# Kernel optimization log

Measured on AMD Instinct MI355X. Metric: run time of the kernel, lower is better.

Reference implementation:

```python
import jax, jax.numpy as jnp
import numpy as np

N = 250000           # points
B = 2                # batch size
GX, GY, GZ = 256, 256, 32   # voxel grid
SCALES = (2, 4, 6, 8)
CIN = 64             # input_channels
CR = 64              # reduce_channels
CH = CR // 2         # hidden = reduce_channels // 2
COUT = 64            # output_channels


def _cdiv(a, b):
    return -(-a // b)


def setup_inputs() -> dict:
    key = jax.random.key(0)
    ks = jax.random.split(key, 16)
    x = jax.random.normal(ks[0], (N, CIN), jnp.float32)
    bcol = jax.random.randint(ks[1], (N, 1), 0, B)
    xy = jax.random.randint(ks[2], (N, 2), 0, GX)
    z = jax.random.randint(ks[3], (N, 1), 0, GZ)
    coords = jnp.concatenate([bcol, xy, z], axis=1).astype(jnp.int32)
    coords_inv = jnp.arange(N, dtype=jnp.int32)

    def lin(k, fan_in, shape):
        return jax.random.normal(k, shape, jnp.float32) / np.sqrt(fan_in)

    return {
        "x": x,
        "coords": coords,
        "coords_inv": coords_inv,
        "W_red": lin(ks[4], CIN, (CIN, CR)),
        "b_red": jnp.zeros((CR,), jnp.float32),
        "W_pool": lin(ks[5], CR, (len(SCALES), CR, CH)),   # fc_list
        "b_pool": jnp.zeros((len(SCALES), CH), jnp.float32),
        "W_att": lin(ks[6], CH, (len(SCALES), CH, CH)),    # fcs
        "b_att": jnp.zeros((len(SCALES), CH), jnp.float32),
        "W_z": lin(ks[7], CH, (CH, CH)),                   # self.fc (no bias)
        "W_out": lin(ks[8], CH, (CH, CR)),                 # out_fc (no bias)
        "W_l1": lin(ks[9], 2 * CR, (2 * CR, CR)),          # linear_output[0] (no bias)
        "W_l2": lin(ks[10], CR, (CR, COUT)),               # linear_output[2]
        "b_l2": jnp.zeros((COUT,), jnp.float32),
    }


def reference(x, coords, coords_inv, W_red, b_red, W_pool, b_pool,
              W_att, b_att, W_z, W_out, W_l1, W_l2, b_l2):
    # feature_reduce + ReLU
    red = jax.nn.relu(x @ W_red + b_red)              # [N, CR]
    bidx = coords[:, 0].astype(jnp.int32)
    cxyz = coords[:, 1:]

    outs = []
    for j, ps in enumerate(SCALES):
        gx, gy, gz = _cdiv(GX, ps), _cdiv(GY, ps), _cdiv(GZ, ps)
        q = cxyz // ps                                 # quantized coords
        seg = ((bidx * gx + q[:, 0]) * gy + q[:, 1]) * gz + q[:, 2]
        ns = B * gx * gy * gz
        # scatter_mean over voxels at this scale
        sums = jax.ops.segment_sum(red, seg, num_segments=ns)
        cnt = jax.ops.segment_sum(jnp.ones((N, 1), red.dtype), seg, num_segments=ns)
        fkm = sums / jnp.maximum(cnt, 1.0)             # [ns, CR]
        # per-scale MLP then gather back to points
        att = jax.nn.relu(fkm @ W_pool[j] + b_pool[j])[seg]   # [N, CH]
        outs.append(att)

    sf = jnp.stack(outs, axis=1)                       # [N, S, CH]
    feat_Z = jax.nn.relu(sf.sum(axis=1) @ W_z)         # [N, CH]
    att_vecs = jnp.stack([feat_Z @ W_att[j] + b_att[j] for j in range(len(SCALES))], axis=1)
    att_vecs = jax.nn.sigmoid(att_vecs)                # [N, S, CH]
    scale_features = (sf * att_vecs).sum(axis=1) @ W_out   # [N, CR]
    out_f = jnp.concatenate([red, scale_features], axis=1)  # [N, 2*CR]
    proj = jax.nn.relu(out_f @ W_l1) @ W_l2 + b_l2     # [N, COUT]
    return proj[coords_inv]
```

## Files before the change

kernel.cpp:

```cpp
#include <hip/hip_runtime.h>
#include <hip/hip_bf16.h>

#define SEG1 524288
#define SEG2 589824
#define SEG3 612012
#define SEGT 620204

#define K2B0 8192
#define K2B1 9216
#define K2B2 9563
#define K2BT 9691

#define PYRB12 10968

#define SUMS_OFF 32000000ull
#define CNT_OFF  111386112ull
#define ATT_OFF  113866928ull
#define WQ_OFF   153560064ull

typedef __attribute__((ext_vector_type(8))) __bf16 bf16x8;
typedef __attribute__((ext_vector_type(4))) float  f32x4;

__device__ __forceinline__ float bf2f(unsigned short u) {
    union { unsigned int i; float f; } v; v.i = ((unsigned int)u) << 16; return v.f;
}
__device__ __forceinline__ unsigned short f2bf(float f) {
    union { float f; unsigned int i; } v; v.f = f;
    unsigned int r = v.i + 0x7FFF + ((v.i >> 16) & 1);
    return (unsigned short)(r >> 16);
}
__device__ __forceinline__ void atom_pk_bf16(unsigned int* addr, unsigned int pk) {
    asm volatile("global_atomic_pk_add_bf16 %0, %1, off" :: "v"(addr), "v"(pk) : "memory");
}

__device__ __forceinline__ int seg0_of(int b, int cx, int cy, int cz) {
    return ((b*128 + (cx>>1))*128 + (cy>>1))*16 + (cz>>1);
}
__device__ __forceinline__ void seg4(int b, int cx, int cy, int cz, int* s) {
    s[0] =        ((b*128 + (cx>>1))*128 + (cy>>1))*16 + (cz>>1);
    s[1] = SEG1 + ((b*64  + (cx>>2))*64  + (cy>>2))*8  + (cz>>2);
    s[2] = SEG2 + ((b*43  + (cx/6 ))*43  + (cy/6 ))*6  + (cz/6 );
    s[3] = SEG3 + ((b*32  + (cx>>3))*32  + (cy>>3))*4  + (cz>>3);
}

__global__ __launch_bounds__(256) void k0_wprep(
    const float* __restrict__ W_red, const float* __restrict__ W_pool,
    const float* __restrict__ W_z, const float* __restrict__ W_att,
    const float* __restrict__ W_out, const float* __restrict__ W_l1,
    const float* __restrict__ W_l2, char* __restrict__ wq)
{
    int g = blockIdx.x*256 + threadIdx.x;
    if (g < 4096) {
        int idx = g; int k = idx>>6, c = idx&63;
        int byte = (((c<<7)+(k<<1)) ^ ((c&7)<<4));
        *(unsigned short*)(wq + byte) = f2bf(W_red[idx]);
    } else if (g < 12288) {
        int idx = g - 4096; int j = idx>>11, r2 = idx&2047, k = r2>>5, c = r2&31;
        int byte = j*4096 + (((c<<7)+(k<<1)) ^ ((c&7)<<4));
        *(unsigned short*)(wq + 8192 + byte) = f2bf(W_pool[idx]);
    } else if (g < 13312) {
        int idx = g - 12288; int k = idx>>5, c = idx&31;
        *(unsigned short*)(wq + 24576 + ((k>>3)*32+c)*16 + (k&7)*2) = f2bf(W_z[idx]);
    } else if (g < 17408) {
        int idx = g - 13312; int j = idx>>10, rem = idx&1023, k = rem>>5, c = rem&31;
        *(unsigned short*)(wq + 26624 + j*2048 + ((k>>3)*32+c)*16 + (k&7)*2) = f2bf(W_att[idx]);
    } else if (g < 19456) {
        int idx = g - 17408; int k = idx>>6, c = idx&63;
        *(unsigned short*)(wq + 34816 + ((k>>3)*64+c)*16 + (k&7)*2) = f2bf(W_out[idx]);
    } else if (g < 27648) {
        int idx = g - 19456; int k = idx>>6, c = idx&63;
        int byte = (((c<<8)+(k<<1)) ^ ((c&7)<<4));
        *(unsigned short*)(wq + 38912 + byte) = f2bf(W_l1[idx]);
    } else if (g < 31744) {
        int idx = g - 27648; int k = idx>>6, c = idx&63;
        int byte = (((c<<7)+(k<<1)) ^ ((c&7)<<4));
        *(unsigned short*)(wq + 55296 + byte) = f2bf(W_l2[idx]);
    }
}

__global__ __launch_bounds__(256) void k1_mfma(
    const float* __restrict__ x, const int* __restrict__ coords,
    const char* __restrict__ wq, const float* __restrict__ b_red,
    unsigned int* __restrict__ red32, unsigned int* __restrict__ sums_pk,
    float* __restrict__ cnt, int n)
{
    __shared__ uint4 Ax4[512];
    __shared__ uint4 Bw4[512];
    __shared__ uint4 Rt4[512];
    __shared__ int segl[64];
    char* Ax = (char*)Ax4; char* Bw = (char*)Bw4; char* Rt = (char*)Rt4;

    int t = threadIdx.x;
    int i0 = blockIdx.x * 64;

    if (t < 64) {
        int r = i0 + t;
        if (r < n) {
            int4 cv = *(const int4*)&coords[(size_t)r*4];
            int s0 = seg0_of(cv.x, cv.y, cv.z, cv.w);
            segl[t] = s0;
            unsafeAtomicAdd(&cnt[s0], 1.f);
        } else segl[t] = -1;
    }
    {
        const uint4* src = (const uint4*)wq;
        for (int idx = t; idx < 512; idx += 256) Bw4[idx] = src[idx];
    }
    #pragma unroll
    for (int i2 = 0; i2 < 2; ++i2) {
        int idx = i2*256 + t;
        int row = idx >> 3, kc = idx & 7;
        int r = i0 + row;
        unsigned short u[8];
        if (r < n) {
            float4 v0 = *(const float4*)&x[(size_t)r*64 + kc*8];
            float4 v1 = *(const float4*)&x[(size_t)r*64 + kc*8 + 4];
            u[0]=f2bf(v0.x); u[1]=f2bf(v0.y); u[2]=f2bf(v0.z); u[3]=f2bf(v0.w);
            u[4]=f2bf(v1.x); u[5]=f2bf(v1.y); u[6]=f2bf(v1.z); u[7]=f2bf(v1.w);
        } else {
            #pragma unroll
            for (int q = 0; q < 8; ++q) u[q] = 0;
        }
        int byte = ((row << 7) + (kc << 4)) ^ ((row & 7) << 4);
        *(uint4*)(Ax + byte) = *(const uint4*)u;
    }
    __syncthreads();

    int lane = t & 63, wv = t >> 6;
    int hi = lane >> 4, lo = lane & 15;
    int arow = wv*16 + lo;

    f32x4 acc[4];
    #pragma unroll
    for (int nt = 0; nt < 4; ++nt) acc[nt] = (f32x4){0.f,0.f,0.f,0.f};
    #pragma unroll
    for (int kk = 0; kk < 2; ++kk) {
        int abyte = ((arow << 7) + ((kk*4 + hi) << 4)) ^ ((arow & 7) << 4);
        bf16x8 af = *(const bf16x8*)(Ax + abyte);
        #pragma unroll
        for (int nt = 0; nt < 4; ++nt) {
            int brow = nt*16 + lo;
            int bbyte = ((brow << 7) + ((kk*4 + hi) << 4)) ^ ((brow & 7) << 4);
            bf16x8 bf = *(const bf16x8*)(Bw + bbyte);
            acc[nt] = __builtin_amdgcn_mfma_f32_16x16x32_bf16(af, bf, acc[nt], 0, 0, 0);
        }
    }
    #pragma unroll
    for (int nt = 0; nt < 4; ++nt) {
        int col = nt*16 + lo;
        float bb = b_red[col];
        #pragma unroll
        for (int r = 0; r < 4; ++r) {
            int row = wv*16 + hi*4 + r;
            int byte = ((row << 7) + (col << 1)) ^ ((row & 7) << 4);
            *(unsigned short*)(Rt + byte) = f2bf(fmaxf(acc[nt][r] + bb, 0.f));
        }
    }
    __syncthreads();

    #pragma unroll
    for (int i2 = 0; i2 < 2; ++i2) {
        int idx = i2*256 + t;
        int row = idx >> 3, ck = idx & 7;
        int r = i0 + row;
        if (r < n) {
            int byte = ((row << 7) + (ck << 4)) ^ ((row & 7) << 4);
            *(uint4*)&red32[(size_t)r*32 + ck*4] = *(const uint4*)(Rt + byte);
        }
    }
    {
        int half = t >> 5, c = t & 31;
        #pragma unroll
        for (int i2 = 0; i2 < 8; ++i2) {
            int p = i2*8 + half;
            int s0_ = segl[p];
            if (s0_ >= 0) {
                int byte = ((p << 7) + (c << 2)) ^ ((p & 7) << 4);
                unsigned int pk = *(const unsigned int*)(Rt + byte);
                atom_pk_bf16(&sums_pk[(size_t)s0_*32 + c], pk);
            }
        }
    }
    asm volatile("s_waitcnt vmcnt(0)" ::: "memory");
}

__global__ __launch_bounds__(256) void k_pyramid(
    unsigned int* __restrict__ sums_pk, float* __restrict__ cnt)
{
    int t = threadIdx.x;
    int lane = t & 31;
    int cg = blockIdx.x * 8 + (t >> 5);

    float a0 = 0.f, a1 = 0.f, ca = 0.f;
    int outSeg = -1;

    if (cg < 65536) {
        int r1 = cg;
        int qz = r1 & 7, qy = (r1 >> 3) & 63, qx = (r1 >> 9) & 63, b = r1 >> 15;
        #pragma unroll
        for (int d = 0; d < 8; ++d) {
            int x2 = 2*qx + (d>>2), y2 = 2*qy + ((d>>1)&1), z2 = 2*qz + (d&1);
            int child = ((b*128 + x2)*128 + y2)*16 + z2;
            unsigned int v = sums_pk[(size_t)child*32 + lane];
            a0 += bf2f((unsigned short)(v & 0xffff));
            a1 += bf2f((unsigned short)(v >> 16));
            if (lane == 0) ca += cnt[child];
        }
        outSeg = SEG1 + r1;
    } else {
        int r2 = cg - 65536;
        if (r2 < 22188) {
            int z6 = r2 % 6; int tmp = r2 / 6;
            int y6 = tmp % 43; tmp /= 43;
            int x6 = tmp % 43; int b = tmp / 43;
            for (int dx = 0; dx < 3; ++dx) {
                int x2 = 3*x6 + dx; if (x2 >= 128) break;
                for (int dy = 0; dy < 3; ++dy) {
                    int y2 = 3*y6 + dy; if (y2 >= 128) break;
                    for (int dz = 0; dz < 3; ++dz) {
                        int z2 = 3*z6 + dz; if (z2 >= 16) break;
                        int child = ((b*128 + x2)*128 + y2)*16 + z2;
                        unsigned int v = sums_pk[(size_t)child*32 + lane];
                        a0 += bf2f((unsigned short)(v & 0xffff));
                        a1 += bf2f((unsigned short)(v >> 16));
                        if (lane == 0) ca += cnt[child];
                    }
                }
            }
            outSeg = SEG2 + r2;
        }
    }

    if (outSeg >= 0) {
        unsigned int pk = (unsigned int)f2bf(a0) | ((unsigned int)f2bf(a1) << 16);
        sums_pk[(size_t)outSeg*32 + lane] = pk;
        if (lane == 0) cnt[outSeg] = ca;
    }
}

__global__ __launch_bounds__(256) void k_pyr3(
    unsigned int* __restrict__ sums_pk, float* __restrict__ cnt)
{
    int t = threadIdx.x;
    int lane = t & 31;
    int r3 = blockIdx.x * 8 + (t >> 5);
    int z8 = r3 & 3, y8 = (r3 >> 2) & 31, x8 = (r3 >> 7) & 31, b = r3 >> 12;
    float a0 = 0.f, a1 = 0.f, ca = 0.f;
    #pragma unroll
    for (int d = 0; d < 8; ++d) {
        int qx = 2*x8 + (d>>2), qy = 2*y8 + ((d>>1)&1), qz = 2*z8 + (d&1);
        int child = SEG1 + ((b*64 + qx)*64 + qy)*8 + qz;
        unsigned int v = sums_pk[(size_t)child*32 + lane];
        a0 += bf2f((unsigned short)(v & 0xffff));
        a1 += bf2f((unsigned short)(v >> 16));
        if (lane == 0) ca += cnt[child];
    }
    unsigned int pk = (unsigned int)f2bf(a0) | ((unsigned int)f2bf(a1) << 16);
    sums_pk[(size_t)(SEG3 + r3)*32 + lane] = pk;
    if (lane == 0) cnt[SEG3 + r3] = ca;
}

__global__ __launch_bounds__(256) void k2_mfma(
    const unsigned int* __restrict__ sums_pk, const float* __restrict__ cnt,
    const char* __restrict__ wq, const float* __restrict__ b_pool,
    unsigned short* __restrict__ att)
{
    __shared__ uint4 As4[512];
    __shared__ uint4 Bs4[256];
    char* As = (char*)As4; char* Bs = (char*)Bs4;

    int t = threadIdx.x;
    int bid = blockIdx.x;
    int j, rel;
    if (bid < K2B0)      { j = 0; rel = bid; }
    else if (bid < K2B1) { j = 1; rel = bid - K2B0; }
    else if (bid < K2B2) { j = 2; rel = bid - K2B1; }
    else                 { j = 3; rel = bid - K2B2; }
    const int segStartT[4] = {0, SEG1, SEG2, SEG3};
    const int segEndT[4]   = {SEG1, SEG2, SEG3, SEGT};
    int s0 = segStartT[j] + rel * 64;
    int sEnd = segEndT[j];

    {
        const uint4* src = (const uint4*)(wq + 8192 + j*4096);
        for (int idx = t; idx < 256; idx += 256) Bs4[idx] = src[idx];
    }
    #pragma unroll
    for (int i = 0; i < 4; ++i) {
        int idx = i*256 + t;
        int p = idx >> 4, c4 = idx & 15;
        int s = s0 + p;
        unsigned int lo = 0, hi2 = 0; float inv = 0.f;
        if (s < sEnd) {
            uint2 v = *(const uint2*)&sums_pk[(size_t)s*32 + c4*2];
            lo = v.x; hi2 = v.y;
            inv = 1.f / fmaxf(cnt[s], 1.f);
        }
        unsigned short u[4] = { f2bf(bf2f((unsigned short)(lo & 0xffff))*inv),
                                f2bf(bf2f((unsigned short)(lo >> 16))*inv),
                                f2bf(bf2f((unsigned short)(hi2 & 0xffff))*inv),
                                f2bf(bf2f((unsigned short)(hi2 >> 16))*inv) };
        int byte = ((p << 7) + (c4 << 3)) ^ ((p & 7) << 4);
        *(uint2*)(As + byte) = *(const uint2*)u;
    }
    __syncthreads();

    int lane = t & 63, wv = t >> 6;
    int hi = lane >> 4, lo = lane & 15;
    int arow = wv*16 + lo;

    f32x4 acc[2];
    acc[0] = (f32x4){0.f,0.f,0.f,0.f};
    acc[1] = (f32x4){0.f,0.f,0.f,0.f};
    #pragma unroll
    for (int kk = 0; kk < 2; ++kk) {
        int abyte = ((arow << 7) + ((kk*4 + hi) << 4)) ^ ((arow & 7) << 4);
        bf16x8 af = *(const bf16x8*)(As + abyte);
        #pragma unroll
        for (int nt = 0; nt < 2; ++nt) {
            int brow = nt*16 + lo;
            int bbyte = ((brow << 7) + ((kk*4 + hi) << 4)) ^ ((brow & 7) << 4);
            bf16x8 bf = *(const bf16x8*)(Bs + bbyte);
            acc[nt] = __builtin_amdgcn_mfma_f32_16x16x32_bf16(af, bf, acc[nt], 0, 0, 0);
        }
    }
    #pragma unroll
    for (int nt = 0; nt < 2; ++nt) {
        int col = nt*16 + lo;
        float bp = b_pool[j*32 + col];
        #pragma unroll
        for (int r = 0; r < 4; ++r) {
            int s = s0 + wv*16 + hi*4 + r;
            if (s < sEnd) att[(size_t)s*32 + col] = f2bf(fmaxf(acc[nt][r] + bp, 0.f));
        }
    }
}

__global__ __launch_bounds__(256) void k3a_mfma(
    const int* __restrict__ coords, const unsigned short* __restrict__ att,
    const char* __restrict__ wq, const float* __restrict__ b_att,
    unsigned short* __restrict__ sfeat, int n)
{
    __shared__ uint4 wcomb4[896];
    __shared__ unsigned short sf[8192];
    __shared__ unsigned short AsWs[2048];
    __shared__ unsigned short Fz[2048];
    __shared__ int segl[64][4];
    char* wzp  = (char*)wcomb4;
    char* wattp = (char*)wcomb4 + 2048;
    char* wotp = (char*)wcomb4 + 10240;

    int t = threadIdx.x;
    int i0 = blockIdx.x * 64;
    if (t < 64) {
        int r = i0 + t; if (r >= n) r = n - 1;
        int sg[4]; seg4(coords[r*4], coords[r*4+1], coords[r*4+2], coords[r*4+3], sg);
        segl[t][0]=sg[0]; segl[t][1]=sg[1]; segl[t][2]=sg[2]; segl[t][3]=sg[3];
    }
    {
        const uint4* src = (const uint4*)(wq + 24576);
        for (int idx = t; idx < 896; idx += 256) wcomb4[idx] = src[idx];
    }
    __syncthreads();

    #pragma unroll
    for (int i = 0; i < 4; ++i) {
        int idx = i*256 + t;
        int p = idx >> 4, j = (idx >> 2) & 3, ck = idx & 3;
        int s = segl[p][j];
        uint4 v = *(const uint4*)(att + (size_t)s*32 + ck*8);
        int off = (j*64 + ck*16) ^ (((p>>2)&3) << 4);
        *(uint4*)((char*)sf + p*256 + off) = v;
        unsigned int w_[4] = {v.x, v.y, v.z, v.w};
        float f[8];
        #pragma unroll
        for (int q = 0; q < 4; ++q) {
            f[2*q]   = bf2f((unsigned short)(w_[q] & 0xffff));
            f[2*q+1] = bf2f((unsigned short)(w_[q] >> 16));
        }
        #pragma unroll
        for (int q = 0; q < 8; ++q) {
            f[q] += __shfl_xor(f[q], 4);
            f[q] += __shfl_xor(f[q], 8);
        }
        if (j == 0) {
            unsigned short u8[8];
            #pragma unroll
            for (int q = 0; q < 8; ++q) u8[q] = f2bf(f[q]);
            *(uint4*)((char*)AsWs + (ck*64 + p)*16) = *(const uint4*)u8;
        }
    }
    __syncthreads();

    int lane = t & 63, wv = t >> 6;
    int hi = lane >> 4, lo = lane & 15;
    int arow = wv*16 + lo;

    {
        bf16x8 af = *(const bf16x8*)((char*)AsWs + (hi*64 + arow)*16);
        f32x4 d0 = (f32x4){0.f,0.f,0.f,0.f}, d1 = (f32x4){0.f,0.f,0.f,0.f};
        bf16x8 b0 = *(const bf16x8*)(wzp + (hi*32 + lo)*16);
        bf16x8 b1 = *(const bf16x8*)(wzp + (hi*32 + 16 + lo)*16);
        d0 = __builtin_amdgcn_mfma_f32_16x16x32_bf16(af, b0, d0, 0,0,0);
        d1 = __builtin_amdgcn_mfma_f32_16x16x32_bf16(af, b1, d1, 0,0,0);
        #pragma unroll
        for (int r = 0; r < 4; ++r) {
            int row = wv*16 + hi*4 + r;
            int c0 = lo, c1 = 16 + lo;
            *(unsigned short*)((char*)Fz + ((c0>>3)*64 + row)*16 + (c0&7)*2) = f2bf(fmaxf(d0[r], 0.f));
            *(unsigned short*)((char*)Fz + ((c1>>3)*64 + row)*16 + (c1&7)*2) = f2bf(fmaxf(d1[r], 0.f));
        }
    }
    __syncthreads();
    {
        float wacc[2][4] = {{0.f,0.f,0.f,0.f},{0.f,0.f,0.f,0.f}};
        bf16x8 af = *(const bf16x8*)((char*)Fz + (hi*64 + arow)*16);
        #pragma unroll
        for (int j = 0; j < 4; ++j) {
            f32x4 d0 = (f32x4){0.f,0.f,0.f,0.f}, d1 = (f32x4){0.f,0.f,0.f,0.f};
            bf16x8 b0 = *(const bf16x8*)(wattp + j*2048 + (hi*32 + lo)*16);
            bf16x8 b1 = *(const bf16x8*)(wattp + j*2048 + (hi*32 + 16 + lo)*16);
            d0 = __builtin_amdgcn_mfma_f32_16x16x32_bf16(af, b0, d0, 0,0,0);
            d1 = __builtin_amdgcn_mfma_f32_16x16x32_bf16(af, b1, d1, 0,0,0);
            float ba0 = b_att[j*32 + lo], ba1 = b_att[j*32 + 16 + lo];
            #pragma unroll
            for (int r = 0; r < 4; ++r) {
                int row = wv*16 + hi*4 + r;
                float s0 = 1.f / (1.f + __expf(-(d0[r] + ba0)));
                float s1 = 1.f / (1.f + __expf(-(d1[r] + ba1)));
                float v0 = bf2f(*(const unsigned short*)((char*)sf + row*256 + ((j*64 + lo*2) ^ (hi<<4))));
                float v1 = bf2f(*(const unsigned short*)((char*)sf + row*256 + ((j*64 + (16+lo)*2) ^ (hi<<4))));
                wacc[0][r] += v0 * s0;
                wacc[1][r] += v1 * s1;
            }
        }
        __syncthreads();
        #pragma unroll
        for (int nt = 0; nt < 2; ++nt) {
            int col = nt*16 + lo;
            #pragma unroll
            for (int r = 0; r < 4; ++r) {
                int row = wv*16 + hi*4 + r;
                *(unsigned short*)((char*)AsWs + ((col>>3)*64 + row)*16 + (col&7)*2) = f2bf(wacc[nt][r]);
            }
        }
    }
    __syncthreads();
    {
        bf16x8 af = *(const bf16x8*)((char*)AsWs + (hi*64 + arow)*16);
        #pragma unroll
        for (int nt = 0; nt < 4; ++nt) {
            f32x4 d = (f32x4){0.f,0.f,0.f,0.f};
            bf16x8 bf = *(const bf16x8*)(wotp + (hi*64 + nt*16 + lo)*16);
            d = __builtin_amdgcn_mfma_f32_16x16x32_bf16(af, bf, d, 0,0,0);
            int col = nt*16 + lo;
            #pragma unroll
            for (int r = 0; r < 4; ++r) {
                int row = i0 + wv*16 + hi*4 + r;
                if (row < n) sfeat[(size_t)row*64 + col] = f2bf(d[r]);
            }
        }
    }
}

__global__ __launch_bounds__(256) void k3b_mfma(
    const int* __restrict__ cinv,
    const unsigned short* __restrict__ red, const unsigned short* __restrict__ sfeat,
    const char* __restrict__ wq, const float* __restrict__ b_l2,
    float* __restrict__ out, int n)
{
    __shared__ uint4 ofs4[1024];
    __shared__ uint4 wl4[1536];
    __shared__ uint4 hs4[512];
    __shared__ int rl[64];
    char* ofs = (char*)ofs4;
    char* wl1 = (char*)wl4;
    char* wl2 = (char*)wl4 + 16384;
    char* hs  = (char*)hs4;

    int t = threadIdx.x;
    int i0 = blockIdx.x * 64;
    if (t < 64) { int i = i0 + t; rl[t] = cinv[(i < n) ? i : (n-1)]; }

    {
        const uint4* src = (const uint4*)(wq + 38912);
        for (int idx = t; idx < 1536; idx += 256) wl4[idx] = src[idx];
    }
    __syncthreads();
    for (int idx = t; idx < 1024; idx += 256) {
        int p = idx >> 4, c = idx & 15;
        int r = rl[p];
        const unsigned short* src = (c < 8) ? (red + (size_t)r*64 + c*8)
                                            : (sfeat + (size_t)r*64 + (c-8)*8);
        uint4 v = *(const uint4*)src;
        int byte = ((p << 8) + (c << 4)) ^ ((p & 7) << 4);
        *(uint4*)(ofs + byte) = v;
    }
    __syncthreads();

    int lane = t & 63, wv = t >> 6;
    int hi = lane >> 4, lo = lane & 15;
    int arow = wv*16 + lo;

    f32x4 acc[4];
    #pragma unroll
    for (int nt = 0; nt < 4; ++nt) acc[nt] = (f32x4){0.f,0.f,0.f,0.f};
    #pragma unroll
    for (int kk = 0; kk < 4; ++kk) {
        int abyte = ((arow << 8) + ((kk*4 + hi) << 4)) ^ ((arow & 7) << 4);
        bf16x8 af = *(const bf16x8*)(ofs + abyte);
        #pragma unroll
        for (int nt = 0; nt < 4; ++nt) {
            int brow = nt*16 + lo;
            int bbyte = ((brow << 8) + ((kk*4 + hi) << 4)) ^ ((brow & 7) << 4);
            bf16x8 bf = *(const bf16x8*)(wl1 + bbyte);
            acc[nt] = __builtin_amdgcn_mfma_f32_16x16x32_bf16(af, bf, acc[nt], 0, 0, 0);
        }
    }
    #pragma unroll
    for (int nt = 0; nt < 4; ++nt) {
        #pragma unroll
        for (int r = 0; r < 4; ++r) {
            int row = wv*16 + hi*4 + r;
            int col = nt*16 + lo;
            int byte = ((row << 7) + (col << 1)) ^ ((row & 7) << 4);
            *(unsigned short*)(hs + byte) = f2bf(fmaxf(acc[nt][r], 0.f));
        }
    }
    __syncthreads();

    f32x4 acc2[4];
    #pragma unroll
    for (int nt = 0; nt < 4; ++nt) acc2[nt] = (f32x4){0.f,0.f,0.f,0.f};
    #pragma unroll
    for (int kk = 0; kk < 2; ++kk) {
        int abyte = ((arow << 7) + ((kk*4 + hi) << 4)) ^ ((arow & 7) << 4);
        bf16x8 af = *(const bf16x8*)(hs + abyte);
        #pragma unroll
        for (int nt = 0; nt < 4; ++nt) {
            int brow = nt*16 + lo;
            int bbyte = ((brow << 7) + ((kk*4 + hi) << 4)) ^ ((brow & 7) << 4);
            bf16x8 bf = *(const bf16x8*)(wl2 + bbyte);
            acc2[nt] = __builtin_amdgcn_mfma_f32_16x16x32_bf16(af, bf, acc2[nt], 0, 0, 0);
        }
    }
    #pragma unroll
    for (int nt = 0; nt < 4; ++nt) {
        int col = nt*16 + lo;
        float bl = b_l2[col];
        #pragma unroll
        for (int r = 0; r < 4; ++r) {
            int row = i0 + wv*16 + hi*4 + r;
            if (row < n) out[(size_t)row*64 + col] = acc2[nt][r] + bl;
        }
    }
}

extern "C" void kernel_launch(void* const* d_in, const int* in_sizes, int n_in,
                              void* d_out, int out_size, void* d_ws, size_t ws_size,
                              hipStream_t stream) {
    const float* x      = (const float*)d_in[0];
    const int*   coords = (const int*)  d_in[1];
    const int*   cinv   = (const int*)  d_in[2];
    const float* W_red  = (const float*)d_in[3];
    const float* b_red  = (const float*)d_in[4];
    const float* W_pool = (const float*)d_in[5];
    const float* b_pool = (const float*)d_in[6];
    const float* W_att  = (const float*)d_in[7];
    const float* b_att  = (const float*)d_in[8];
    const float* W_z    = (const float*)d_in[9];
    const float* W_out  = (const float*)d_in[10];
    const float* W_l1   = (const float*)d_in[11];
    const float* W_l2   = (const float*)d_in[12];
    const float* b_l2   = (const float*)d_in[13];
    float* out = (float*)d_out;
    int n = in_sizes[0] / 64;

    char* wsb = (char*)d_ws;
    unsigned int*   red32   = (unsigned int*)(wsb);
    unsigned short* red     = (unsigned short*)(wsb);
    unsigned int*   sums_pk = (unsigned int*)(wsb + SUMS_OFF);
    float*          cnt     = (float*)(wsb + CNT_OFF);
    unsigned short* att     = (unsigned short*)(wsb + ATT_OFF);
    char*           wq      = wsb + WQ_OFF;
    unsigned short* sfeat   = (unsigned short*)(wsb + SUMS_OFF);

    k0_wprep<<<124, 256, 0, stream>>>(W_red, W_pool, W_z, W_att, W_out, W_l1, W_l2, wq);
    hipMemsetAsync(sums_pk, 0, (size_t)SEG1 * 128ull, stream);
    hipMemsetAsync(cnt, 0, (size_t)SEG1 * 4ull, stream);

    k1_mfma<<<(n + 63) / 64, 256, 0, stream>>>(x, coords, wq, b_red, red32, sums_pk, cnt, n);
    k_pyramid<<<PYRB12, 256, 0, stream>>>(sums_pk, cnt);
    k_pyr3<<<1024, 256, 0, stream>>>(sums_pk, cnt);
    k2_mfma<<<K2BT, 256, 0, stream>>>(sums_pk, cnt, wq, b_pool, att);
    k3a_mfma<<<(n + 63) / 64, 256, 0, stream>>>(coords, att, wq, b_att, sfeat, n);
    k3b_mfma<<<(n + 63) / 64, 256, 0, stream>>>(cinv, red, sfeat, wq, b_l2, out, n);
}
```

Measured before the change: 228.4 us.

## Fuse attention and output MLP kernels, skip empty voxels in pyramid and pool

```diff
diff --git a/kernel.cpp b/kernel.cpp
--- a/kernel.cpp
+++ b/kernel.cpp
@@ -201,10 +201,13 @@
         for (int d = 0; d < 8; ++d) {
             int x2 = 2*qx + (d>>2), y2 = 2*qy + ((d>>1)&1), z2 = 2*qz + (d&1);
             int child = ((b*128 + x2)*128 + y2)*16 + z2;
-            unsigned int v = sums_pk[(size_t)child*32 + lane];
-            a0 += bf2f((unsigned short)(v & 0xffff));
-            a1 += bf2f((unsigned short)(v >> 16));
-            if (lane == 0) ca += cnt[child];
+            float cc = cnt[child];
+            if (cc > 0.f) {
+                unsigned int v = sums_pk[(size_t)child*32 + lane];
+                a0 += bf2f((unsigned short)(v & 0xffff));
+                a1 += bf2f((unsigned short)(v >> 16));
+                ca += cc;
+            }
         }
         outSeg = SEG1 + r1;
     } else {
@@ -220,10 +223,13 @@
                     for (int dz = 0; dz < 3; ++dz) {
                         int z2 = 3*z6 + dz; if (z2 >= 16) break;
                         int child = ((b*128 + x2)*128 + y2)*16 + z2;
-                        unsigned int v = sums_pk[(size_t)child*32 + lane];
-                        a0 += bf2f((unsigned short)(v & 0xffff));
-                        a1 += bf2f((unsigned short)(v >> 16));
-                        if (lane == 0) ca += cnt[child];
+                        float cc = cnt[child];
+                        if (cc > 0.f) {
+                            unsigned int v = sums_pk[(size_t)child*32 + lane];
+                            a0 += bf2f((unsigned short)(v & 0xffff));
+                            a1 += bf2f((unsigned short)(v >> 16));
+                            ca += cc;
+                        }
                     }
                 }
             }
@@ -290,12 +296,13 @@
         int idx = i*256 + t;
         int p = idx >> 4, c4 = idx & 15;
         int s = s0 + p;
-        unsigned int lo = 0, hi2 = 0; float inv = 0.f;
-        if (s < sEnd) {
+        unsigned int lo = 0, hi2 = 0; float cv = 0.f;
+        if (s < sEnd) cv = cnt[s];
+        if (cv > 0.f) {
             uint2 v = *(const uint2*)&sums_pk[(size_t)s*32 + c4*2];
             lo = v.x; hi2 = v.y;
-            inv = 1.f / fmaxf(cnt[s], 1.f);
-        }
+        }
+        float inv = (cv > 0.f) ? 1.f / cv : 0.f;
         unsigned short u[4] = { f2bf(bf2f((unsigned short)(lo & 0xffff))*inv),
                                 f2bf(bf2f((unsigned short)(lo >> 16))*inv),
                                 f2bf(bf2f((unsigned short)(hi2 & 0xffff))*inv),
@@ -331,35 +338,48 @@
         #pragma unroll
         for (int r = 0; r < 4; ++r) {
             int s = s0 + wv*16 + hi*4 + r;
-            if (s < sEnd) att[(size_t)s*32 + col] = f2bf(fmaxf(acc[nt][r] + bp, 0.f));
-        }
-    }
-}
-
-__global__ __launch_bounds__(256) void k3a_mfma(
-    const int* __restrict__ coords, const unsigned short* __restrict__ att,
+            if (s < sEnd && cnt[s] > 0.f)
+                att[(size_t)s*32 + col] = f2bf(fmaxf(acc[nt][r] + bp, 0.f));
+        }
+    }
+}
+
+#define SF_O   0
+#define WZ_O   16384
+#define WATT_O 18432
+#define WL2_O  16384
+#define WOT_O  26624
+#define ASWS_O 30720
+#define FZ_O   34816
+#define HS_O   30720
+#define OFS_O  38912
+#define SEGL_O 55296
+#define RL_O   56320
+__global__ __launch_bounds__(256) void k3_fused(
+    const int* __restrict__ coords, const int* __restrict__ cinv,
+    const unsigned short* __restrict__ att, const unsigned short* __restrict__ red,
     const char* __restrict__ wq, const float* __restrict__ b_att,
-    unsigned short* __restrict__ sfeat, int n)
+    const float* __restrict__ b_l2, float* __restrict__ out, int n)
 {
-    __shared__ uint4 wcomb4[896];
-    __shared__ unsigned short sf[8192];
-    __shared__ unsigned short AsWs[2048];
-    __shared__ unsigned short Fz[2048];
-    __shared__ int segl[64][4];
-    char* wzp  = (char*)wcomb4;
-    char* wattp = (char*)wcomb4 + 2048;
-    char* wotp = (char*)wcomb4 + 10240;
+    __shared__ uint4 L4[3536];
+    char* L = (char*)L4;
+    int* segl = (int*)(L + SEGL_O);
+    int* rl   = (int*)(L + RL_O);
 
     int t = threadIdx.x;
     int i0 = blockIdx.x * 64;
+
     if (t < 64) {
-        int r = i0 + t; if (r >= n) r = n - 1;
+        int i = i0 + t;
+        int r = cinv[(i < n) ? i : (n - 1)];
+        rl[t] = r;
         int sg[4]; seg4(coords[r*4], coords[r*4+1], coords[r*4+2], coords[r*4+3], sg);
-        segl[t][0]=sg[0]; segl[t][1]=sg[1]; segl[t][2]=sg[2]; segl[t][3]=sg[3];
+        segl[t*4+0]=sg[0]; segl[t*4+1]=sg[1]; segl[t*4+2]=sg[2]; segl[t*4+3]=sg[3];
     }
     {
         const uint4* src = (const uint4*)(wq + 24576);
-        for (int idx = t; idx < 896; idx += 256) wcomb4[idx] = src[idx];
+        uint4* dst = (uint4*)(L + WZ_O);
+        for (int idx = t; idx < 896; idx += 256) dst[idx] = src[idx];
     }
     __syncthreads();
 
@@ -367,10 +387,10 @@
     for (int i = 0; i < 4; ++i) {
         int idx = i*256 + t;
         int p = idx >> 4, j = (idx >> 2) & 3, ck = idx & 3;
-        int s = segl[p][j];
+        int s = segl[p*4+j];
         uint4 v = *(const uint4*)(att + (size_t)s*32 + ck*8);
         int off = (j*64 + ck*16) ^ (((p>>2)&3) << 4);
-        *(uint4*)((char*)sf + p*256 + off) = v;
+        *(uint4*)(L + SF_O + p*256 + off) = v;
         unsigned int w_[4] = {v.x, v.y, v.z, v.w};
         float f[8];
         #pragma unroll
@@ -387,8 +407,17 @@
             unsigned short u8[8];
             #pragma unroll
             for (int q = 0; q < 8; ++q) u8[q] = f2bf(f[q]);
-            *(uint4*)((char*)AsWs + (ck*64 + p)*16) = *(const uint4*)u8;
-        }
+            *(uint4*)(L + ASWS_O + (ck*64 + p)*16) = *(const uint4*)u8;
+        }
+    }
+    #pragma unroll
+    for (int i = 0; i < 2; ++i) {
+        int idx = i*256 + t;
+        int p = idx >> 3, c = idx & 7;
+        int r = rl[p];
+        uint4 v = *(const uint4*)(red + (size_t)r*64 + c*8);
+        int byte = ((p << 8) + (c << 4)) ^ ((p & 7) << 4);
+        *(uint4*)(L + OFS_O + byte) = v;
     }
     __syncthreads();
 
@@ -397,29 +426,29 @@
     int arow = wv*16 + lo;
 
     {
-        bf16x8 af = *(const bf16x8*)((char*)AsWs + (hi*64 + arow)*16);
+        bf16x8 af = *(const bf16x8*)(L + ASWS_O + (hi*64 + arow)*16);
         f32x4 d0 = (f32x4){0.f,0.f,0.f,0.f}, d1 = (f32x4){0.f,0.f,0.f,0.f};
-        bf16x8 b0 = *(const bf16x8*)(wzp + (hi*32 + lo)*16);
-        bf16x8 b1 = *(const bf16x8*)(wzp + (hi*32 + 16 + lo)*16);
+        bf16x8 b0 = *(const bf16x8*)(L + WZ_O + (hi*32 + lo)*16);
+        bf16x8 b1 = *(const bf16x8*)(L + WZ_O + (hi*32 + 16 + lo)*16);
         d0 = __builtin_amdgcn_mfma_f32_16x16x32_bf16(af, b0, d0, 0,0,0);
         d1 = __builtin_amdgcn_mfma_f32_16x16x32_bf16(af, b1, d1, 0,0,0);
         #pragma unroll
         for (int r = 0; r < 4; ++r) {
             int row = wv*16 + hi*4 + r;
             int c0 = lo, c1 = 16 + lo;
-            *(unsigned short*)((char*)Fz + ((c0>>3)*64 + row)*16 + (c0&7)*2) = f2bf(fmaxf(d0[r], 0.f));
-            *(unsigned short*)((char*)Fz + ((c1>>3)*64 + row)*16 + (c1&7)*2) = f2bf(fmaxf(d1[r], 0.f));
+            *(unsigned short*)(L + FZ_O + ((c0>>3)*64 + row)*16 + (c0&7)*2) = f2bf(fmaxf(d0[r], 0.f));
+            *(unsigned short*)(L + FZ_O + ((c1>>3)*64 + row)*16 + (c1&7)*2) = f2bf(fmaxf(d1[r], 0.f));
         }
     }
     __syncthreads();
     {
         float wacc[2][4] = {{0.f,0.f,0.f,0.f},{0.f,0.f,0.f,0.f}};
-        bf16x8 af = *(const bf16x8*)((char*)Fz + (hi*64 + arow)*16);
+        bf16x8 af = *(const bf16x8*)(L + FZ_O + (hi*64 + arow)*16);
         #pragma unroll
         for (int j = 0; j < 4; ++j) {
             f32x4 d0 = (f32x4){0.f,0.f,0.f,0.f}, d1 = (f32x4){0.f,0.f,0.f,0.f};
-            bf16x8 b0 = *(const bf16x8*)(wattp + j*2048 + (hi*32 + lo)*16);
-            bf16x8 b1 = *(const bf16x8*)(wattp + j*2048 + (hi*32 + 16 + lo)*16);
+            bf16x8 b0 = *(const bf16x8*)(L + WATT_O + j*2048 + (hi*32 + lo)*16);
+            bf16x8 b1 = *(const bf16x8*)(L + WATT_O + j*2048 + (hi*32 + 16 + lo)*16);
             d0 = __builtin_amdgcn_mfma_f32_16x16x32_bf16(af, b0, d0, 0,0,0);
             d1 = __builtin_amdgcn_mfma_f32_16x16x32_bf16(af, b1, d1, 0,0,0);
             float ba0 = b_att[j*32 + lo], ba1 = b_att[j*32 + 16 + lo];
@@ -428,8 +457,8 @@
                 int row = wv*16 + hi*4 + r;
                 float s0 = 1.f / (1.f + __expf(-(d0[r] + ba0)));
                 float s1 = 1.f / (1.f + __expf(-(d1[r] + ba1)));
-                float v0 = bf2f(*(const unsigned short*)((char*)sf + row*256 + ((j*64 + lo*2) ^ (hi<<4))));
-                float v1 = bf2f(*(const unsigned short*)((char*)sf + row*256 + ((j*64 + (16+lo)*2) ^ (hi<<4))));
+                float v0 = bf2f(*(const unsigned short*)(L + SF_O + row*256 + ((j*64 + lo*2) ^ (hi<<4))));
+                float v1 = bf2f(*(const unsigned short*)(L + SF_O + row*256 + ((j*64 + (16+lo)*2) ^ (hi<<4))));
                 wacc[0][r] += v0 * s0;
                 wacc[1][r] += v1 * s1;
             }
@@ -441,66 +470,35 @@
             #pragma unroll
             for (int r = 0; r < 4; ++r) {
                 int row = wv*16 + hi*4 + r;
-                *(unsigned short*)((char*)AsWs + ((col>>3)*64 + row)*16 + (col&7)*2) = f2bf(wacc[nt][r]);
+                *(unsigned short*)(L + ASWS_O + ((col>>3)*64 + row)*16 + (col&7)*2) = f2bf(wacc[nt][r]);
             }
         }
     }
     __syncthreads();
     {
-        bf16x8 af = *(const bf16x8*)((char*)AsWs + (hi*64 + arow)*16);
+        const uint4* src1 = (const uint4*)(wq + 38912);
+        uint4* dst1 = (uint4*)(L + SF_O);
+        for (int idx = t; idx < 1024; idx += 256) dst1[idx] = src1[idx];
+        const uint4* src2 = (const uint4*)(wq + 55296);
+        uint4* dst2 = (uint4*)(L + WL2_O);
+        for (int idx = t; idx < 512; idx += 256) dst2[idx] = src2[idx];
+
+        bf16x8 af = *(const bf16x8*)(L + ASWS_O + (hi*64 + arow)*16);
         #pragma unroll
         for (int nt = 0; nt < 4; ++nt) {
             f32x4 d = (f32x4){0.f,0.f,0.f,0.f};
-            bf16x8 bf = *(const bf16x8*)(wotp + (hi*64 + nt*16 + lo)*16);
+            bf16x8 bf = *(const bf16x8*)(L + WOT_O + (hi*64 + nt*16 + lo)*16);
             d = __builtin_amdgcn_mfma_f32_16x16x32_bf16(af, bf, d, 0,0,0);
-            int col = nt*16 + lo;
+            int col2 = 64 + nt*16 + lo;
             #pragma unroll
             for (int r = 0; r < 4; ++r) {
-                int row = i0 + wv*16 + hi*4 + r;
-                if (row < n) sfeat[(size_t)row*64 + col] = f2bf(d[r]);
+                int row = wv*16 + hi*4 + r;
+                int byte = (((row << 8) + (col2 << 1)) ^ ((row & 7) << 4));
+                *(unsigned short*)(L + OFS_O + byte) = f2bf(d[r]);
             }
         }
     }
-}
-
-__global__ __launch_bounds__(256) void k3b_mfma(
-    const int* __restrict__ cinv,
-    const unsigned short* __restrict__ red, const unsigned short* __restrict__ sfeat,
-    const char* __restrict__ wq, const float* __restrict__ b_l2,
-    float* __restrict__ out, int n)
-{
-    __shared__ uint4 ofs4[1024];
-    __shared__ uint4 wl4[1536];
-    __shared__ uint4 hs4[512];
-    __shared__ int rl[64];
-    char* ofs = (char*)ofs4;
-    char* wl1 = (char*)wl4;
-    char* wl2 = (char*)wl4 + 16384;
-    char* hs  = (char*)hs4;
-
-    int t = threadIdx.x;
-    int i0 = blockIdx.x * 64;
-    if (t < 64) { int i = i0 + t; rl[t] = cinv[(i < n) ? i : (n-1)]; }
-
-    {
-        const uint4* src = (const uint4*)(wq + 38912);
-        for (int idx = t; idx < 1536; idx += 256) wl4[idx] = src[idx];
-    }
-    __syncthreads();
-    for (int idx = t; idx < 1024; idx += 256) {
-        int p = idx >> 4, c = idx & 15;
-        int r = rl[p];
-        const unsigned short* src = (c < 8) ? (red + (size_t)r*64 + c*8)
-                                            : (sfeat + (size_t)r*64 + (c-8)*8);
-        uint4 v = *(const uint4*)src;
-        int byte = ((p << 8) + (c << 4)) ^ ((p & 7) << 4);
-        *(uint4*)(ofs + byte) = v;
-    }
-    __syncthreads();
-
-    int lane = t & 63, wv = t >> 6;
-    int hi = lane >> 4, lo = lane & 15;
-    int arow = wv*16 + lo;
+    __syncthreads();
 
     f32x4 acc[4];
     #pragma unroll
@@ -508,12 +506,12 @@
     #pragma unroll
     for (int kk = 0; kk < 4; ++kk) {
         int abyte = ((arow << 8) + ((kk*4 + hi) << 4)) ^ ((arow & 7) << 4);
-        bf16x8 af = *(const bf16x8*)(ofs + abyte);
+        bf16x8 af = *(const bf16x8*)(L + OFS_O + abyte);
         #pragma unroll
         for (int nt = 0; nt < 4; ++nt) {
             int brow = nt*16 + lo;
             int bbyte = ((brow << 8) + ((kk*4 + hi) << 4)) ^ ((brow & 7) << 4);
-            bf16x8 bf = *(const bf16x8*)(wl1 + bbyte);
+            bf16x8 bf = *(const bf16x8*)(L + SF_O + bbyte);
             acc[nt] = __builtin_amdgcn_mfma_f32_16x16x32_bf16(af, bf, acc[nt], 0, 0, 0);
         }
     }
@@ -524,7 +522,7 @@
             int row = wv*16 + hi*4 + r;
             int col = nt*16 + lo;
             int byte = ((row << 7) + (col << 1)) ^ ((row & 7) << 4);
-            *(unsigned short*)(hs + byte) = f2bf(fmaxf(acc[nt][r], 0.f));
+            *(unsigned short*)(L + HS_O + byte) = f2bf(fmaxf(acc[nt][r], 0.f));
         }
     }
     __syncthreads();
@@ -535,12 +533,12 @@
     #pragma unroll
     for (int kk = 0; kk < 2; ++kk) {
         int abyte = ((arow << 7) + ((kk*4 + hi) << 4)) ^ ((arow & 7) << 4);
-        bf16x8 af = *(const bf16x8*)(hs + abyte);
+        bf16x8 af = *(const bf16x8*)(L + HS_O + abyte);
         #pragma unroll
         for (int nt = 0; nt < 4; ++nt) {
             int brow = nt*16 + lo;
             int bbyte = ((brow << 7) + ((kk*4 + hi) << 4)) ^ ((brow & 7) << 4);
-            bf16x8 bf = *(const bf16x8*)(wl2 + bbyte);
+            bf16x8 bf = *(const bf16x8*)(L + WL2_O + bbyte);
             acc2[nt] = __builtin_amdgcn_mfma_f32_16x16x32_bf16(af, bf, acc2[nt], 0, 0, 0);
         }
     }
@@ -583,7 +581,6 @@
     float*          cnt     = (float*)(wsb + CNT_OFF);
     unsigned short* att     = (unsigned short*)(wsb + ATT_OFF);
     char*           wq      = wsb + WQ_OFF;
-    unsigned short* sfeat   = (unsigned short*)(wsb + SUMS_OFF);
 
     k0_wprep<<<124, 256, 0, stream>>>(W_red, W_pool, W_z, W_att, W_out, W_l1, W_l2, wq);
     hipMemsetAsync(sums_pk, 0, (size_t)SEG1 * 128ull, stream);
@@ -593,6 +590,5 @@
     k_pyramid<<<PYRB12, 256, 0, stream>>>(sums_pk, cnt);
     k_pyr3<<<1024, 256, 0, stream>>>(sums_pk, cnt);
     k2_mfma<<<K2BT, 256, 0, stream>>>(sums_pk, cnt, wq, b_pool, att);
-    k3a_mfma<<<(n + 63) / 64, 256, 0, stream>>>(coords, att, wq, b_att, sfeat, n);
-    k3b_mfma<<<(n + 63) / 64, 256, 0, stream>>>(cinv, red, sfeat, wq, b_l2, out, n);
-}
+    k3_fused<<<(n + 63) / 64, 256, 0, stream>>>(coords, cinv, att, red, wq, b_att, b_l2, out, n);
+}
```

New measurement: 257.4 us. 1.13x slower.
